# Optimization experiments

Hardware: AMD Instinct MI355X
Metric: run time of the kernel (lower is better)

## Reference

```python
import jax, jax.numpy as jnp
import numpy as np

G_CRYSTALS = 64   # number of crystals in the batch
N_ATOMS = 64      # atoms per crystal (dense n^2 edge block per crystal)
N_HEADS = 8
HEAD_DIM = 64


def _make_edges(g, n):
    # dense all-pairs (i, j) within each crystal; atoms of crystal c occupy [c*n, (c+1)*n)
    base = np.arange(g, dtype=np.int32)[:, None, None] * n   # (G,1,1)
    idx = np.arange(n, dtype=np.int32)
    e0 = np.broadcast_to(base + idx[None, :, None], (g, n, n)).reshape(-1)  # query index
    e1 = np.broadcast_to(base + idx[None, None, :], (g, n, n)).reshape(-1)  # key index
    return jnp.asarray(np.stack([e0, e1], axis=0))  # (2, M)


def setup_inputs() -> dict:
    key = jax.random.key(0)
    k0, k1, k2, k3, k4 = jax.random.split(key, 5)
    N = G_CRYSTALS * N_ATOMS                 # 4096 atoms total
    M = G_CRYSTALS * N_ATOMS * N_ATOMS       # 262144 edges
    q = jax.random.normal(k0, (N, N_HEADS, HEAD_DIM), jnp.float32)
    k = jax.random.normal(k1, (N, N_HEADS, HEAD_DIM), jnp.float32)
    v = jax.random.normal(k2, (N, N_HEADS, HEAD_DIM), jnp.float32)
    attn_weights = jax.random.normal(k3, (M, N_HEADS), jnp.float32)          # per-edge additive bias
    values = jax.random.normal(k4, (M, N_HEADS, HEAD_DIM), jnp.float32) * 0.1  # per-edge fused value term
    edges = _make_edges(G_CRYSTALS, N_ATOMS)
    return {"q": q, "k": k, "v": v, "attn_weights": attn_weights,
            "values": values, "edges": edges}


def reference(q, k, v, attn_weights, values, edges):
    # Faithful to the norm_func_mode==0 ('default') fallback path of
    # _scaled_dot_product_attention: per-edge logits, softmax over keys per
    # query (within each crystal's dense block), fused value term.
    N, H, Dh = q.shape
    e0, e1 = edges[0], edges[1]
    scale = 1.0 / jnp.sqrt(jnp.asarray(Dh, q.dtype))
    # per-edge attention logits: (M, H)
    a = jnp.einsum('mhd,mhd->mh', q[e0] * scale, k[e1]) + attn_weights
    # stable softmax over edges sharing the same query index e0
    m = jax.ops.segment_max(a, e0, num_segments=N)      # (N, H)
    p = jnp.exp(a - m[e0])                              # (M, H)
    denom = jax.ops.segment_sum(p, e0, num_segments=N)  # (N, H)
    w = p / denom[e0]                                   # (M, H)
    # output[i] = sum_j w[ij] * (v[j] + values[ij])
    out = jax.ops.segment_sum(w[:, :, None] * (v[e1] + values), e0, num_segments=N)
    return out  # (N, H, Dh)
```

## Files before the change

### kernel.cpp

```cpp
#include <hip/hip_runtime.h>


#define NH 8
#define HD 64
#define ROWSTRIDE 68

__global__ __launch_bounds__(256, 2)
void crystal_attn_kernel(const float* __restrict__ q,
                         const float* __restrict__ k,
                         const float* __restrict__ v,
                         const float* __restrict__ aw,
                         const float* __restrict__ values,
                         float* __restrict__ out) {
    const int c = blockIdx.x & 63;
    const int h = blockIdx.x >> 6;
    const int t = threadIdx.x;

    __shared__ __align__(16) float sq[64][ROWSTRIDE];
    __shared__ __align__(16) float sk[64][ROWSTRIDE];
    __shared__ __align__(16) float sv[64][ROWSTRIDE];
    __shared__ __align__(16) float sa[64][ROWSTRIDE];
    __shared__ float sden[64];

    {
        const size_t rowbase = ((size_t)c * 64) * (NH * HD) + (size_t)h * HD;
        const float* qg = q + rowbase;
        const float* kg = k + rowbase;
        const float* vg = v + rowbase;
        #pragma unroll
        for (int s = 0; s < 4; ++s) {
            int u   = t + 256 * s;
            int row = u >> 4;
            int col = (u & 15) * 4;
            size_t goff = (size_t)row * (NH * HD) + col;
            *(float4*)&sq[row][col] = *(const float4*)(qg + goff);
            *(float4*)&sk[row][col] = *(const float4*)(kg + goff);
            *(float4*)&sv[row][col] = *(const float4*)(vg + goff);
        }
        const float* ag = aw + ((size_t)c * 4096) * NH + h;
        #pragma unroll
        for (int s = 0; s < 16; ++s) {
            int idx = t + 256 * s;
            sa[idx >> 6][idx & 63] = ag[(size_t)idx * NH];
        }
    }
    __syncthreads();

    {
        const int w = t >> 6;
        const int i = t & 63;
        const int jbase = w * 16;
        float acc[16];
        #pragma unroll
        for (int jj = 0; jj < 16; ++jj) acc[jj] = 0.f;
        #pragma unroll 4
        for (int d4 = 0; d4 < 16; ++d4) {
            float4 qv = *(const float4*)&sq[i][d4 * 4];
            #pragma unroll
            for (int jj = 0; jj < 16; ++jj) {
                float4 kv = *(const float4*)&sk[jbase + jj][d4 * 4];
                acc[jj] += qv.x * kv.x + qv.y * kv.y + qv.z * kv.z + qv.w * kv.w;
            }
        }
        #pragma unroll
        for (int jj = 0; jj < 16; ++jj)
            sa[i][jbase + jj] = acc[jj] * 0.125f + sa[i][jbase + jj];
    }
    __syncthreads();

    {
        const int r  = t >> 2;
        const int jb = (t & 3) * 16;
        float mx = -1e30f;
        #pragma unroll
        for (int jj = 0; jj < 16; ++jj) mx = fmaxf(mx, sa[r][jb + jj]);
        mx = fmaxf(mx, __shfl_xor(mx, 1));
        mx = fmaxf(mx, __shfl_xor(mx, 2));
        float sum = 0.f;
        #pragma unroll
        for (int jj = 0; jj < 16; ++jj) {
            float p = __expf(sa[r][jb + jj] - mx);
            sa[r][jb + jj] = p;
            sum += p;
        }
        sum += __shfl_xor(sum, 1);
        sum += __shfl_xor(sum, 2);
        if ((t & 3) == 0) sden[r] = sum;
    }
    __syncthreads();

    {
        const int w    = t >> 6;
        const int lane = t & 63;
        const int e    = lane >> 4;
        const int dq   = lane & 15;
        const float* vb = values + ((size_t)c * 4096) * (NH * HD) + (size_t)h * HD + dq * 4;
        float* ob = out + ((size_t)c * 64) * (NH * HD) + (size_t)h * HD + dq * 4;
        #pragma unroll
        for (int r = 0; r < 4; ++r) {
            const int i = 16 * w + 4 * r + e;
            const float* vrow = vb + (size_t)i * 64 * (NH * HD);
            float4 acc = make_float4(0.f, 0.f, 0.f, 0.f);
            #pragma unroll 8
            for (int j = 0; j < 64; ++j) {
                float4 val = *(const float4*)(vrow + (size_t)j * (NH * HD));
                float  p   = sa[i][j];
                float4 sj  = *(const float4*)&sv[j][dq * 4];
                acc.x += p * (sj.x + val.x);
                acc.y += p * (sj.y + val.y);
                acc.z += p * (sj.z + val.z);
                acc.w += p * (sj.w + val.w);
            }
            const float inv = 1.0f / sden[i];
            float4 o = make_float4(acc.x * inv, acc.y * inv, acc.z * inv, acc.w * inv);
            *(float4*)(ob + (size_t)i * (NH * HD)) = o;
        }
    }
}

extern "C" void kernel_launch(void* const* d_in, const int* in_sizes, int n_in,
                              void* d_out, int out_size, void* d_ws, size_t ws_size,
                              hipStream_t stream) {
    const float* q      = (const float*)d_in[0];
    const float* k      = (const float*)d_in[1];
    const float* v      = (const float*)d_in[2];
    const float* aw     = (const float*)d_in[3];
    const float* values = (const float*)d_in[4];
    float* out = (float*)d_out;

    dim3 grid(512);
    dim3 block(256);
    hipLaunchKernelGGL(crystal_attn_kernel, grid, block, 0, stream,
                       q, k, v, aw, values, out);
}
```

Baseline: 709.4 us.

## Split attention into softmax kernel and fully coalesced values-streaming kernel

The fused kernel is split in two. The first kernel computes the normalized softmax weights per crystal and head and writes them to workspace. The second kernel streams the large per-edge values tensor with one block per (crystal, query atom) across all heads, so each edge row is read as contiguous 2 KB chunks, replacing strided 256-byte reads, with many more blocks in flight. The cost is an extra global round trip for the weights (about 8 MB), a second launch, and v being reread once per query.

```diff
diff --git a/kernel.cpp b/kernel.cpp
--- a/kernel.cpp
+++ b/kernel.cpp
@@ -5,28 +5,23 @@
 #define HD 64
 #define ROWSTRIDE 68
 
-__global__ __launch_bounds__(256, 2)
-void crystal_attn_kernel(const float* __restrict__ q,
-                         const float* __restrict__ k,
-                         const float* __restrict__ v,
-                         const float* __restrict__ aw,
-                         const float* __restrict__ values,
-                         float* __restrict__ out) {
+__global__ __launch_bounds__(256, 3)
+void softmax_kernel(const float* __restrict__ q,
+                    const float* __restrict__ k,
+                    const float* __restrict__ aw,
+                    float* __restrict__ w_out) {
     const int c = blockIdx.x & 63;
     const int h = blockIdx.x >> 6;
     const int t = threadIdx.x;
 
     __shared__ __align__(16) float sq[64][ROWSTRIDE];
     __shared__ __align__(16) float sk[64][ROWSTRIDE];
-    __shared__ __align__(16) float sv[64][ROWSTRIDE];
     __shared__ __align__(16) float sa[64][ROWSTRIDE];
-    __shared__ float sden[64];
 
     {
         const size_t rowbase = ((size_t)c * 64) * (NH * HD) + (size_t)h * HD;
         const float* qg = q + rowbase;
         const float* kg = k + rowbase;
-        const float* vg = v + rowbase;
         #pragma unroll
         for (int s = 0; s < 4; ++s) {
             int u   = t + 256 * s;
@@ -35,7 +30,6 @@
             size_t goff = (size_t)row * (NH * HD) + col;
             *(float4*)&sq[row][col] = *(const float4*)(qg + goff);
             *(float4*)&sk[row][col] = *(const float4*)(kg + goff);
-            *(float4*)&sv[row][col] = *(const float4*)(vg + goff);
         }
         const float* ag = aw + ((size_t)c * 4096) * NH + h;
         #pragma unroll
@@ -47,9 +41,9 @@
     __syncthreads();
 
     {
-        const int w = t >> 6;
-        const int i = t & 63;
-        const int jbase = w * 16;
+        const int wv = t >> 6;
+        const int i  = t & 63;
+        const int jbase = wv * 16;
         float acc[16];
         #pragma unroll
         for (int jj = 0; jj < 16; ++jj) acc[jj] = 0.f;
@@ -71,50 +65,80 @@
     {
         const int r  = t >> 2;
         const int jb = (t & 3) * 16;
+        float p[16];
         float mx = -1e30f;
         #pragma unroll
-        for (int jj = 0; jj < 16; ++jj) mx = fmaxf(mx, sa[r][jb + jj]);
+        for (int jj = 0; jj < 16; ++jj) { p[jj] = sa[r][jb + jj]; mx = fmaxf(mx, p[jj]); }
         mx = fmaxf(mx, __shfl_xor(mx, 1));
         mx = fmaxf(mx, __shfl_xor(mx, 2));
         float sum = 0.f;
         #pragma unroll
-        for (int jj = 0; jj < 16; ++jj) {
-            float p = __expf(sa[r][jb + jj] - mx);
-            sa[r][jb + jj] = p;
-            sum += p;
-        }
+        for (int jj = 0; jj < 16; ++jj) { p[jj] = __expf(p[jj] - mx); sum += p[jj]; }
         sum += __shfl_xor(sum, 1);
         sum += __shfl_xor(sum, 2);
-        if ((t & 3) == 0) sden[r] = sum;
+        const float inv = 1.0f / sum;
+        float* wg = w_out + ((size_t)(c * NH + h)) * 4096 + r * 64 + jb;
+        #pragma unroll
+        for (int s = 0; s < 4; ++s) {
+            float4 o = make_float4(p[4*s] * inv, p[4*s+1] * inv,
+                                   p[4*s+2] * inv, p[4*s+3] * inv);
+            *(float4*)(wg + 4 * s) = o;
+        }
+    }
+}
+
+__global__ __launch_bounds__(256, 8)
+void stream_kernel(const float* __restrict__ v,
+                   const float* __restrict__ values,
+                   const float* __restrict__ w_in,
+                   float* __restrict__ out) {
+    const int c = blockIdx.x & 63;
+    const int i = blockIdx.x >> 6;
+    const int t = threadIdx.x;
+
+    __shared__ float sw[NH][64];
+    __shared__ float sred[4][512];
+
+    #pragma unroll
+    for (int s = 0; s < 2; ++s) {
+        int idx = t + 256 * s;
+        sw[idx >> 6][idx & 63] =
+            w_in[((size_t)(c * NH) + (idx >> 6)) * 4096 + i * 64 + (idx & 63)];
     }
     __syncthreads();
 
-    {
-        const int w    = t >> 6;
-        const int lane = t & 63;
-        const int e    = lane >> 4;
-        const int dq   = lane & 15;
-        const float* vb = values + ((size_t)c * 4096) * (NH * HD) + (size_t)h * HD + dq * 4;
-        float* ob = out + ((size_t)c * 64) * (NH * HD) + (size_t)h * HD + dq * 4;
-        #pragma unroll
-        for (int r = 0; r < 4; ++r) {
-            const int i = 16 * w + 4 * r + e;
-            const float* vrow = vb + (size_t)i * 64 * (NH * HD);
-            float4 acc = make_float4(0.f, 0.f, 0.f, 0.f);
-            #pragma unroll 8
-            for (int j = 0; j < 64; ++j) {
-                float4 val = *(const float4*)(vrow + (size_t)j * (NH * HD));
-                float  p   = sa[i][j];
-                float4 sj  = *(const float4*)&sv[j][dq * 4];
-                acc.x += p * (sj.x + val.x);
-                acc.y += p * (sj.y + val.y);
-                acc.z += p * (sj.z + val.z);
-                acc.w += p * (sj.w + val.w);
-            }
-            const float inv = 1.0f / sden[i];
-            float4 o = make_float4(acc.x * inv, acc.y * inv, acc.z * inv, acc.w * inv);
-            *(float4*)(ob + (size_t)i * (NH * HD)) = o;
-        }
+    const int ww = t >> 6;
+    const int l  = t & 63;
+    const int jbase = ww * 16;
+    const int h0 = l >> 4;
+    const float* valbase = values + ((size_t)(c * 4096 + i * 64 + jbase)) * 512;
+    const float* vbase   = v      + ((size_t)(c * 64 + jbase)) * 512;
+
+    float4 acc0 = make_float4(0.f, 0.f, 0.f, 0.f);
+    float4 acc1 = make_float4(0.f, 0.f, 0.f, 0.f);
+    #pragma unroll 4
+    for (int jj = 0; jj < 16; ++jj) {
+        const size_t ro = (size_t)jj * 512 + 4 * l;
+        float4 a0 = *(const float4*)(valbase + ro);
+        float4 a1 = *(const float4*)(valbase + ro + 256);
+        float4 b0 = *(const float4*)(vbase + ro);
+        float4 b1 = *(const float4*)(vbase + ro + 256);
+        float w0 = sw[h0][jbase + jj];
+        float w1 = sw[h0 + 4][jbase + jj];
+        acc0.x += w0 * (b0.x + a0.x); acc0.y += w0 * (b0.y + a0.y);
+        acc0.z += w0 * (b0.z + a0.z); acc0.w += w0 * (b0.w + a0.w);
+        acc1.x += w1 * (b1.x + a1.x); acc1.y += w1 * (b1.y + a1.y);
+        acc1.z += w1 * (b1.z + a1.z); acc1.w += w1 * (b1.w + a1.w);
+    }
+    *(float4*)&sred[ww][4 * l]       = acc0;
+    *(float4*)&sred[ww][256 + 4 * l] = acc1;
+    __syncthreads();
+
+    float* ob = out + ((size_t)(c * 64 + i)) * 512;
+    #pragma unroll
+    for (int s = 0; s < 2; ++s) {
+        int d = t + 256 * s;
+        ob[d] = sred[0][d] + sred[1][d] + sred[2][d] + sred[3][d];
     }
 }
 
@@ -127,9 +151,10 @@
     const float* aw     = (const float*)d_in[3];
     const float* values = (const float*)d_in[4];
     float* out = (float*)d_out;
+    float* w_ws = (float*)d_ws;
 
-    dim3 grid(512);
-    dim3 block(256);
-    hipLaunchKernelGGL(crystal_attn_kernel, grid, block, 0, stream,
-                       q, k, v, aw, values, out);
+    hipLaunchKernelGGL(softmax_kernel, dim3(512), dim3(256), 0, stream,
+                       q, k, aw, w_ws);
+    hipLaunchKernelGGL(stream_kernel, dim3(4096), dim3(256), 0, stream,
+                       v, values, w_ws, out);
 }
```

New measurement: 730.8 us. 3.0% more time.
